# Optimization experiments

Hardware: AMD Instinct MI355X
Metric: run time of the kernel (lower is better)

The kernel has to match this reference:

```python
import jax, jax.numpy as jnp
import numpy as np

K_NN = 3  # pointnet2 relation default k=3


def setup_inputs() -> dict:
    key = jax.random.key(0)
    k1, k2, k3 = jax.random.split(key, 3)
    B, N, S, C = 4, 16384, 4096, 256
    q = jax.random.normal(k1, (B, N, 3), dtype=jnp.float32)
    k = jax.random.normal(k2, (B, S, 3), dtype=jnp.float32)
    v = jax.random.normal(k3, (B, S, C), dtype=jnp.float32)
    return {"q": q, "k": k, "v": v}


def reference(q, k, v):
    # squared pairwise distance: ||q||^2 - 2 q.k + ||k||^2  -> [B, N, S]
    d = (
        jnp.sum(q * q, axis=-1, keepdims=True)
        - 2.0 * jnp.einsum("bnd,bsd->bns", q, k)
        + jnp.sum(k * k, axis=-1)[:, None, :]
    )
    # 3 nearest neighbors (smallest distances)
    neg_d, idx = jax.lax.top_k(-d, K_NN)          # [B, N, 3]
    dists = -neg_d
    recip = 1.0 / (dists + 1e-8)
    weight = recip / jnp.sum(recip, axis=-1, keepdims=True)  # [B, N, 3]
    # score is zero except at idx; scatter+dense matmul == gather-weighted sum
    B = q.shape[0]
    vg = v[jnp.arange(B)[:, None, None], idx]     # [B, N, 3, C]
    extract = jnp.einsum("bnk,bnkc->bnc", weight, vg)  # [B, N, C]
    return jnp.transpose(extract, (0, 2, 1))      # [B, C, N] (embed is identity)
```

## Files before the change

### kernel.cpp

```cpp
#include <hip/hip_runtime.h>

#define BB 4
#define NN 16384
#define SS 4096
#define CC 256
#define TLD 132

typedef float f32x4 __attribute__((ext_vector_type(4)));

__device__ __forceinline__ bool lexlt(float da, int ia, float db, int ib) {
  return (da < db) || ((da == db) && (ia < ib));
}

#define DIST(kp) ({                                        \
  float _dot = (qx * (kp).x + qy * (kp).y) + qz * (kp).z;  \
  __builtin_fmaf(_dot, -2.0f, qq) + (kp).w;                \
})

#define INSERT(dd, ss) do {                                \
  bool _k2 = (dd) < d2, _k1 = (dd) < d1, _k0 = (dd) < d0;  \
  float _nd2 = __builtin_amdgcn_fmed3f((dd), d1, d2);      \
  float _nd1 = __builtin_amdgcn_fmed3f((dd), d0, d1);      \
  float _nd0 = fminf((dd), d0);                            \
  i2 = _k1 ? i1 : (_k2 ? (ss) : i2);                       \
  i1 = _k0 ? i0 : (_k1 ? (ss) : i1);                       \
  i0 = _k0 ? (ss) : i0;                                    \
  d2 = _nd2; d1 = _nd1; d0 = _nd0;                         \
} while (0)

__global__ __launch_bounds__(256, 4) void scan_kernel(
    const float* __restrict__ qg, const float* __restrict__ kg,
    float4* __restrict__ dpart, int4* __restrict__ ipart) {
#pragma clang fp contract(off)
  __shared__ __align__(16) float4 kpts[1024];

  const int tid = threadIdx.x;
  const int blk = blockIdx.x;
  const int b = blk >> 8;
  const int seg = (blk >> 6) & 3;
  const int n0 = (blk & 63) << 8;
  const int wv = tid >> 6;
  const int lane = tid & 63;
  const int q = n0 + wv * 64 + lane;

  {
    const float* kb = kg + ((long)b * SS + (long)seg * 1024) * 3;
    const float4* src = (const float4*)kb + tid * 3;
    float4 f0 = src[0], f1 = src[1], f2 = src[2];
    float px[4] = {f0.x, f0.w, f1.z, f2.y};
    float py[4] = {f0.y, f1.x, f1.w, f2.z};
    float pz[4] = {f0.z, f1.y, f2.x, f2.w};
#pragma unroll
    for (int m = 0; m < 4; ++m) {
      float kk = (px[m] * px[m] + py[m] * py[m]) + pz[m] * pz[m];
      kpts[tid * 4 + m] = make_float4(px[m], py[m], pz[m], kk);
    }
  }

  const float* qp = qg + ((long)b * NN + q) * 3;
  float qx = qp[0], qy = qp[1], qz = qp[2];
  float qq = (qx * qx + qy * qy) + qz * qz;
  float d0 = 3.4e38f, d1 = 3.4e38f, d2 = 3.4e38f;
  int i0 = 0, i1 = 0, i2 = 0;
  __syncthreads();

  const int sb = seg * 1024;

  for (int bdl = 0; bdl < 16; ++bdl) {
    const int base = bdl << 4;
    float dv[16];
#pragma unroll
    for (int sj = 0; sj < 4; ++sj) {
      float4 ka = kpts[base + 4 * sj + 0];
      float4 kb_ = kpts[base + 4 * sj + 1];
      float4 kc = kpts[base + 4 * sj + 2];
      float4 kd = kpts[base + 4 * sj + 3];
      dv[4 * sj + 0] = DIST(ka);
      dv[4 * sj + 1] = DIST(kb_);
      dv[4 * sj + 2] = DIST(kc);
      dv[4 * sj + 3] = DIST(kd);
    }
#pragma unroll
    for (int j = 0; j < 16; ++j) INSERT(dv[j], sb + base + j);
  }

  for (int bdl = 16; bdl < 64; ++bdl) {
    const int base = bdl << 4;
    const float tau = d2;
    float dv[16];
    unsigned msk = 0;
#pragma unroll
    for (int sj = 0; sj < 4; ++sj) {
      float4 ka = kpts[base + 4 * sj + 0];
      float4 kb_ = kpts[base + 4 * sj + 1];
      float4 kc = kpts[base + 4 * sj + 2];
      float4 kd = kpts[base + 4 * sj + 3];
      dv[4 * sj + 0] = DIST(ka);
      dv[4 * sj + 1] = DIST(kb_);
      dv[4 * sj + 2] = DIST(kc);
      dv[4 * sj + 3] = DIST(kd);
    }
#pragma unroll
    for (int j = 0; j < 16; ++j) msk |= (__any(dv[j] < tau) ? 1u : 0u) << j;
    if (msk) {
#pragma unroll
      for (int j = 0; j < 16; ++j) {
        if (msk & (1u << j)) INSERT(dv[j], sb + base + j);
      }
    }
  }

  long gid = (long)b * NN + q;
  dpart[gid * 4 + seg] = make_float4(d0, d1, d2, 0.0f);
  ipart[gid * 4 + seg] = make_int4(i0, i1, i2, 0);
}

__global__ __launch_bounds__(256, 4) void gather_kernel(
    const float* __restrict__ vg, const float4* __restrict__ dpart,
    const int4* __restrict__ ipart, float* __restrict__ outg) {
#pragma clang fp contract(off)
  __shared__ __align__(16) float tile[64 * TLD];
  __shared__ float sw[64][3];
  __shared__ int si[64][3];

  const int tid = threadIdx.x;
  const int bid = blockIdx.x;
  const int xcd = bid & 7;
  const int b = xcd >> 1;
  const int chunk = xcd & 1;
  const int nblk = bid >> 3;
  const int n0 = nblk << 6;

  if (tid < 64) {
    long gid = (long)b * NN + n0 + tid;
    float D0 = 3.4e38f, D1 = 3.4e38f, D2 = 3.4e38f;
    int I0 = -1, I1 = -1, I2 = -1;
#pragma unroll
    for (int seg = 0; seg < 4; ++seg) {
      float4 dv = dpart[gid * 4 + seg];
      int4 iv = ipart[gid * 4 + seg];
      float ds_[3] = {dv.x, dv.y, dv.z};
      int is_[3] = {iv.x, iv.y, iv.z};
      for (int r = 0; r < 3; ++r) {
        float d = ds_[r];
        int s = is_[r];
        if (lexlt(d, s, D2, I2)) {
          if (lexlt(d, s, D1, I1)) {
            D2 = D1; I2 = I1;
            if (lexlt(d, s, D0, I0)) { D1 = D0; I1 = I0; D0 = d; I0 = s; }
            else { D1 = d; I1 = s; }
          } else { D2 = d; I2 = s; }
        }
      }
    }
    float r0 = 1.0f / (D0 + 1e-8f);
    float r1 = 1.0f / (D1 + 1e-8f);
    float r2 = 1.0f / (D2 + 1e-8f);
    float rs = (r0 + r1) + r2;
    sw[tid][0] = r0 / rs; sw[tid][1] = r1 / rs; sw[tid][2] = r2 / rs;
    si[tid][0] = I0; si[tid][1] = I1; si[tid][2] = I2;
  }
  __syncthreads();

  const int wv = tid >> 6;
  const int lane = tid & 63;
  const int qh = lane >> 5;
  const int slot = lane & 31;
  const float* vb = vg + (long)b * SS * CC + chunk * 128;

#pragma unroll 4
  for (int it = 0; it < 8; ++it) {
    int qs = wv * 16 + it * 2 + qh;
    float w0 = sw[qs][0], w1 = sw[qs][1], w2 = sw[qs][2];
    const float4* r0p = (const float4*)(vb + (long)si[qs][0] * CC);
    const float4* r1p = (const float4*)(vb + (long)si[qs][1] * CC);
    const float4* r2p = (const float4*)(vb + (long)si[qs][2] * CC);
    float4 a0 = r0p[slot], a1 = r1p[slot], a2 = r2p[slot];
    float4 acc;
    acc.x = (w0 * a0.x + w1 * a1.x) + w2 * a2.x;
    acc.y = (w0 * a0.y + w1 * a1.y) + w2 * a2.y;
    acc.z = (w0 * a0.z + w1 * a1.z) + w2 * a2.z;
    acc.w = (w0 * a0.w + w1 * a1.w) + w2 * a2.w;
    *(float4*)&tile[qs * TLD + slot * 4] = acc;
  }
  __syncthreads();

  {
    const int nf = tid & 15;
    const int cb0 = tid >> 4;
    const int q0 = nf << 2;
#pragma unroll 2
    for (int it = 0; it < 8; ++it) {
      int cl = cb0 + it * 16;
      int cch = (chunk << 7) + cl;
      f32x4 val;
      val.x = tile[(q0 + 0) * TLD + cl];
      val.y = tile[(q0 + 1) * TLD + cl];
      val.z = tile[(q0 + 2) * TLD + cl];
      val.w = tile[(q0 + 3) * TLD + cl];
      __builtin_nontemporal_store(
          val, (f32x4*)&outg[((long)(b * CC + cch)) * NN + n0 + q0]);
    }
  }
}

extern "C" void kernel_launch(void* const* d_in, const int* in_sizes, int n_in,
                              void* d_out, int out_size, void* d_ws, size_t ws_size,
                              hipStream_t stream) {
  const float* q = (const float*)d_in[0];
  const float* k = (const float*)d_in[1];
  const float* v = (const float*)d_in[2];
  float* out = (float*)d_out;
  float4* dpart = (float4*)d_ws;
  int4* ipart = (int4*)((char*)d_ws + (size_t)BB * NN * 4 * 16);
  hipLaunchKernelGGL(scan_kernel, dim3(1024), dim3(256), 0, stream, q, k, dpart, ipart);
  hipLaunchKernelGGL(gather_kernel, dim3(2048), dim3(256), 0, stream, v, dpart, ipart, out);
}
```

Measured before the change: 210.5 us.

## Split scan kernel candidate range across wave pairs and merge top-3 in LDS

Each block now handles 128 queries instead of 256. Two wave pairs split the block's 1024 candidate keys in half, and their partial top-3 lists are merged through shared memory, which the kernel reuses by overwriting kpts. The grid doubles to 2048 blocks and launch bounds rise to 8 blocks per CU, aiming for more parallelism and occupancy in the scan. The unconditional warm-up phase is removed, so the skip mask is used from the first block of candidates. Each half-range sees fewer candidates, so its top-3 threshold tightens more slowly and more inserts run. The merge also adds two barriers.

```diff
diff --git a/kernel.cpp b/kernel.cpp
--- a/kernel.cpp
+++ b/kernel.cpp
@@ -28,20 +28,24 @@
   d2 = _nd2; d1 = _nd1; d0 = _nd0;                         \
 } while (0)
 
-__global__ __launch_bounds__(256, 4) void scan_kernel(
+__global__ __launch_bounds__(256, 8) void scan_kernel(
     const float* __restrict__ qg, const float* __restrict__ kg,
     float4* __restrict__ dpart, int4* __restrict__ ipart) {
 #pragma clang fp contract(off)
   __shared__ __align__(16) float4 kpts[1024];
+  float* md = (float*)kpts;
+  int* mi = (int*)((char*)kpts + 1536);
 
   const int tid = threadIdx.x;
   const int blk = blockIdx.x;
-  const int b = blk >> 8;
-  const int seg = (blk >> 6) & 3;
-  const int n0 = (blk & 63) << 8;
+  const int b = blk >> 9;
+  const int seg = (blk >> 7) & 3;
+  const int n0 = (blk & 127) << 7;
   const int wv = tid >> 6;
   const int lane = tid & 63;
-  const int q = n0 + wv * 64 + lane;
+  const int qg2 = wv & 1;
+  const int half = wv >> 1;
+  const int q = n0 + qg2 * 64 + lane;
 
   {
     const float* kb = kg + ((long)b * SS + (long)seg * 1024) * 3;
@@ -65,10 +69,13 @@
   __syncthreads();
 
   const int sb = seg * 1024;
-
-  for (int bdl = 0; bdl < 16; ++bdl) {
-    const int base = bdl << 4;
+  const int cbase = half << 9;
+
+  for (int bdl = 0; bdl < 32; ++bdl) {
+    const int base = cbase + (bdl << 4);
+    const float tau = d2;
     float dv[16];
+    unsigned msk = 0;
 #pragma unroll
     for (int sj = 0; sj < 4; ++sj) {
       float4 ka = kpts[base + 4 * sj + 0];
@@ -81,26 +88,6 @@
       dv[4 * sj + 3] = DIST(kd);
     }
 #pragma unroll
-    for (int j = 0; j < 16; ++j) INSERT(dv[j], sb + base + j);
-  }
-
-  for (int bdl = 16; bdl < 64; ++bdl) {
-    const int base = bdl << 4;
-    const float tau = d2;
-    float dv[16];
-    unsigned msk = 0;
-#pragma unroll
-    for (int sj = 0; sj < 4; ++sj) {
-      float4 ka = kpts[base + 4 * sj + 0];
-      float4 kb_ = kpts[base + 4 * sj + 1];
-      float4 kc = kpts[base + 4 * sj + 2];
-      float4 kd = kpts[base + 4 * sj + 3];
-      dv[4 * sj + 0] = DIST(ka);
-      dv[4 * sj + 1] = DIST(kb_);
-      dv[4 * sj + 2] = DIST(kc);
-      dv[4 * sj + 3] = DIST(kd);
-    }
-#pragma unroll
     for (int j = 0; j < 16; ++j) msk |= (__any(dv[j] < tau) ? 1u : 0u) << j;
     if (msk) {
 #pragma unroll
@@ -110,9 +97,35 @@
     }
   }
 
-  long gid = (long)b * NN + q;
-  dpart[gid * 4 + seg] = make_float4(d0, d1, d2, 0.0f);
-  ipart[gid * 4 + seg] = make_int4(i0, i1, i2, 0);
+  __syncthreads();
+  if (half == 1) {
+    int basei = (qg2 * 64 + lane) * 3;
+    md[basei + 0] = d0; md[basei + 1] = d1; md[basei + 2] = d2;
+    mi[basei + 0] = i0; mi[basei + 1] = i1; mi[basei + 2] = i2;
+  }
+  __syncthreads();
+  if (half == 0) {
+    int basei = (qg2 * 64 + lane) * 3;
+    float E0 = md[basei + 0], E1 = md[basei + 1], E2 = md[basei + 2];
+    int F0 = mi[basei + 0], F1 = mi[basei + 1], F2 = mi[basei + 2];
+    float A0 = d0, A1 = d1, A2 = d2;
+    int B0 = i0, B1 = i1, B2 = i2;
+    bool t = lexlt(E0, F0, A0, B0);
+    float r0 = t ? E0 : A0; int s0 = t ? F0 : B0;
+    float nA0 = t ? A0 : A1, nA1 = t ? A1 : A2;
+    int nB0 = t ? B0 : B1, nB1 = t ? B1 : B2;
+    float nE0 = t ? E1 : E0, nE1 = t ? E2 : E1;
+    int nF0 = t ? F1 : F0, nF1 = t ? F2 : F1;
+    bool u = lexlt(nE0, nF0, nA0, nB0);
+    float r1 = u ? nE0 : nA0; int s1 = u ? nF0 : nB0;
+    float mA0 = u ? nA0 : nA1; int mB0 = u ? nB0 : nB1;
+    float mE0 = u ? nE1 : nE0; int mF0 = u ? nF1 : nF0;
+    bool w = lexlt(mE0, mF0, mA0, mB0);
+    float r2 = w ? mE0 : mA0; int s2 = w ? mF0 : mB0;
+    long gid = (long)b * NN + q;
+    dpart[gid * 4 + seg] = make_float4(r0, r1, r2, 0.0f);
+    ipart[gid * 4 + seg] = make_int4(s0, s1, s2, 0);
+  }
 }
 
 __global__ __launch_bounds__(256, 4) void gather_kernel(
@@ -213,6 +226,6 @@
   float* out = (float*)d_out;
   float4* dpart = (float4*)d_ws;
   int4* ipart = (int4*)((char*)d_ws + (size_t)BB * NN * 4 * 16);
-  hipLaunchKernelGGL(scan_kernel, dim3(1024), dim3(256), 0, stream, q, k, dpart, ipart);
+  hipLaunchKernelGGL(scan_kernel, dim3(2048), dim3(256), 0, stream, q, k, dpart, ipart);
   hipLaunchKernelGGL(gather_kernel, dim3(2048), dim3(256), 0, stream, v, dpart, ipart, out);
 }
```

New measurement: 212.0 us. No clear change (+0.7%).
